# Kernel tuning notes

Measured on AMD Instinct MI355X. Metric: run time of the kernel, lower is better.

## Reference

```python
import jax, jax.numpy as jnp
import numpy as np

_EPS = 1e-6

def _warp_x(images, x_src):
    # images: [B,H,W,C]; x_src: [H,W] source x-coordinate for each output pixel
    # Nearest-neighbor resample along width, zero fill outside (tf ImageProjectiveTransform semantics).
    B, H, W, C = images.shape
    xi = jnp.round(x_src).astype(jnp.int32)
    valid = (xi >= 0) & (xi < W)
    xic = jnp.clip(xi, 0, W - 1)
    row = jnp.broadcast_to(jnp.arange(H)[:, None], (H, W))
    out = images[:, row, xic, :]  # gather -> [B,H,W,C]
    return out * valid[None, :, :, None].astype(images.dtype)

def _shear_x(images, mag):
    # transform matrix [1, mag, 0, 0, 1, 0]: x_in = x + mag * y
    H, W = images.shape[1], images.shape[2]
    yy = jnp.arange(H, dtype=jnp.float32)[:, None]
    xx = jnp.arange(W, dtype=jnp.float32)[None, :]
    return _warp_x(images, xx + mag * yy)

def _translate_x(images, pixels):
    # transform matrix [1, 0, -pixels, 0, 1, 0]: x_in = x - pixels
    H, W = images.shape[1], images.shape[2]
    xx = jnp.broadcast_to(jnp.arange(W, dtype=jnp.float32)[None, :], (H, W))
    return _warp_x(images, xx - pixels)

def _gumbel_softmax_hard(logits, u, tau=1.0):
    g = -jnp.log(-jnp.log(jnp.clip(u, _EPS, 1.0 - _EPS)))
    y = jax.nn.softmax((logits + g) / tau)
    onehot = jax.nn.one_hot(jnp.argmax(y), logits.shape[-1], dtype=y.dtype)
    return jax.lax.stop_gradient(onehot - y) + y  # straight-through hard sample

def _relaxed_bernoulli_hard(p, u, temperature=1.0):
    p = jnp.clip(p, _EPS, 1.0 - _EPS)
    l = jnp.log(jnp.clip(u, _EPS, 1.0 - _EPS)) - jnp.log1p(-jnp.clip(u, _EPS, 1.0 - _EPS))
    y = jax.nn.sigmoid((jnp.log(p) - jnp.log1p(-p) + l) / temperature)
    return jax.lax.stop_gradient(jnp.round(y) - y) + y  # straight-through hard sample

def _apply_bernoulli(x, op_fn, prob, magnitude, u_l):
    hw = _relaxed_bernoulli_hard(prob, u_l)
    x = x + magnitude - jax.lax.stop_gradient(magnitude)  # ST path for magnitude grad
    return jnp.where(hw == 1, op_fn(x, magnitude) * hw, x * (1 - hw))

def _forward(x, sp_weights, sp_probs, sp_magnitudes, u_gumbel, u_logistic):
    # sub-policy j=0: ShearX(-0.3, 0.3); j=1: TranslateX(-10, 10)
    ops = [
        lambda img, m: _shear_x(img, 0.6 * m - 0.3),
        lambda img, m: _translate_x(img, 20.0 * m - 10.0),
    ]
    num_ops, num_sp = sp_weights.shape
    for i in range(num_ops):
        hardwts = _gumbel_softmax_hard(sp_weights[i], u_gumbel[i])
        total = None
        for j in range(num_sp):
            term = jnp.where(
                hardwts[j] == 1,
                _apply_bernoulli(x, ops[j], sp_probs[i, j], sp_magnitudes[i, j], u_logistic[i, j]) * hardwts[j],
                hardwts[j],
            )
            total = term if total is None else total + term
        x = total
    return x

def setup_inputs() -> dict:
    key = jax.random.key(0)
    ks = jax.random.split(key, 6)
    x = jax.random.uniform(ks[0], (256, 224, 224, 3), dtype=jnp.float32)
    sp_weights = jax.random.uniform(ks[1], (2, 2), dtype=jnp.float32)
    sp_probs = jax.random.uniform(ks[2], (2, 2), dtype=jnp.float32)
    sp_magnitudes = jax.random.uniform(ks[3], (2, 2), dtype=jnp.float32)
    u_gumbel = jax.random.uniform(ks[4], (2, 2), dtype=jnp.float32)
    u_logistic = jax.random.uniform(ks[5], (2, 2), dtype=jnp.float32)
    return {"x": x, "sp_weights": sp_weights, "sp_probs": sp_probs,
            "sp_magnitudes": sp_magnitudes, "u_gumbel": u_gumbel, "u_logistic": u_logistic}

def reference(x, sp_weights, sp_probs, sp_magnitudes, u_gumbel, u_logistic):
    return _forward(x, sp_weights, sp_probs, sp_magnitudes, u_gumbel, u_logistic)
```

## Files before the change

kernel.cpp:

```cpp
#include <hip/hip_runtime.h>
#include <math.h>

#define EPS_F 1e-6f
#define CLIP_HI 0.999999f
#define IMG_W 224
#define IMG_H 224
#define ROWF (IMG_W * 3)

typedef float f32x4 __attribute__((ext_vector_type(4)));
typedef float f32x4_u __attribute__((ext_vector_type(4), aligned(4)));

__device__ __forceinline__ float clip01(float u) {
    return fminf(fmaxf(u, EPS_F), CLIP_HI);
}

__global__ void decide_kernel(const float* __restrict__ spw,
                              const float* __restrict__ spp,
                              const float* __restrict__ spm,
                              const float* __restrict__ ug,
                              const float* __restrict__ ul,
                              float* __restrict__ dec) {
    if (threadIdx.x != 0 || blockIdx.x != 0) return;
    for (int i = 0; i < 2; ++i) {
        float g0 = -logf(-logf(clip01(ug[i * 2 + 0])));
        float g1 = -logf(-logf(clip01(ug[i * 2 + 1])));
        int j = (spw[i * 2 + 0] + g0 >= spw[i * 2 + 1] + g1) ? 0 : 1;
        float p = clip01(spp[i * 2 + j]);
        float uc = clip01(ul[i * 2 + j]);
        float l = logf(uc) - log1pf(-uc);
        float s = (logf(p) - log1pf(-p)) + l;
        float y = 1.0f / (1.0f + expf(-s));
        int hw = (int)rintf(y);
        float m = spm[i * 2 + j];
        float active = 0.f, a = 0.f, b = 0.f;
        if (hw == 1) {
            active = 1.f;
            if (j == 0) {
                a = 0.6f * m - 0.3f;
            } else {
                b = -(20.0f * m - 10.0f);
            }
        }
        dec[i * 4 + 0] = active;
        dec[i * 4 + 1] = a;
        dec[i * 4 + 2] = b;
        dec[i * 4 + 3] = m;
    }
}

__global__ __launch_bounds__(256) void warp_kernel(const float* __restrict__ x,
                                                   const float* __restrict__ dec,
                                                   float* __restrict__ out,
                                                   int total_q) {
    int q = blockIdx.x * 256 + threadIdx.x;
    if (q >= total_q) return;
    int pos = q * 4;
    int row = pos / ROWF;
    int within = pos - row * ROWF;
    int h = row % IMG_H;
    int base = row * ROWF;

    const float a0 = dec[1], b0 = dec[2], m0 = dec[3];
    const float a1 = dec[5], b1 = dec[6], m1 = dec[7];
    const float hf = (float)h;
    const float sh1 = a1 * hf + b1;
    const float sh0 = a0 * hf + b0;

    int wA = within / 3;
    int cA = within - wA * 3;

    int x1A = (int)rintf((float)wA + sh1);
    bool vA = (x1A >= 0) && (x1A < IMG_W);
    int x0A = (int)rintf((float)x1A + sh0);
    vA = vA && (x0A >= 0) && (x0A < IMG_W);

    int x1B = (int)rintf((float)(wA + 1) + sh1);
    bool vB = (x1B >= 0) && (x1B < IMG_W);
    int x0B = (int)rintf((float)x1B + sh0);
    vB = vB && (x0B >= 0) && (x0B < IMG_W);

    bool fast = vA && vB && (x0B == x0A + 1);

    float r[4];
    if (__all(fast)) {
        const f32x4_u* src = reinterpret_cast<const f32x4_u*>(&x[base + 3 * x0A + cA]);
        f32x4_u v = *src;
#pragma unroll
        for (int e = 0; e < 4; ++e)
            r[e] = (((v[e] + m0) - m0) + m1) - m1;
    } else {
        int srcs[4];
        bool vs[4];
#pragma unroll
        for (int e = 0; e < 4; ++e) {
            int ce = cA + e;
            bool useB = (ce >= 3);
            int w0 = useB ? x0B : x0A;
            bool v = useB ? vB : vA;
            int cc = useB ? (ce - 3) : ce;
            int w0c = min(max(w0, 0), IMG_W - 1);
            srcs[e] = base + 3 * w0c + cc;
            vs[e] = v;
        }
        float vals[4];
#pragma unroll
        for (int e = 0; e < 4; ++e) vals[e] = x[srcs[e]];
#pragma unroll
        for (int e = 0; e < 4; ++e) {
            float t = vs[e] ? vals[e] : 0.f;
            t = (((t + m0) - m0) + m1) - m1;
            r[e] = vs[e] ? t : 0.f;
        }
    }

    f32x4 o = { r[0], r[1], r[2], r[3] };
    __builtin_nontemporal_store(o, reinterpret_cast<f32x4*>(&out[pos]));
}

extern "C" void kernel_launch(void* const* d_in, const int* in_sizes, int n_in,
                              void* d_out, int out_size, void* d_ws, size_t ws_size,
                              hipStream_t stream) {
    const float* x   = (const float*)d_in[0];
    const float* spw = (const float*)d_in[1];
    const float* spp = (const float*)d_in[2];
    const float* spm = (const float*)d_in[3];
    const float* ug  = (const float*)d_in[4];
    const float* ul  = (const float*)d_in[5];
    float* dec = (float*)d_ws;
    float* out = (float*)d_out;

    decide_kernel<<<1, 1, 0, stream>>>(spw, spp, spm, ug, ul, dec);

    int total_q = out_size / 4;
    int blocks = (total_q + 255) / 256;
    warp_kernel<<<blocks, 256, 0, stream>>>(x, dec, out, total_q);
}
```

Before: 56.71 us.

## Fuse decision computation into warp kernel and process two quads per thread

Removes the separate single-thread decide kernel. Each block's thread 0 now recomputes the sampling decisions into shared memory, followed by a block barrier. Each thread also handles two 4-float groups, one in each half of the output, which halves the grid size. This saves a kernel launch and its serialization, but every block now does redundant transcendental work and waits on a sync. The bounds check is gone, so the output size must divide evenly, which holds for this shape.

```diff
diff --git a/kernel.cpp b/kernel.cpp
--- a/kernel.cpp
+++ b/kernel.cpp
@@ -14,57 +14,17 @@
     return fminf(fmaxf(u, EPS_F), CLIP_HI);
 }
 
-__global__ void decide_kernel(const float* __restrict__ spw,
-                              const float* __restrict__ spp,
-                              const float* __restrict__ spm,
-                              const float* __restrict__ ug,
-                              const float* __restrict__ ul,
-                              float* __restrict__ dec) {
-    if (threadIdx.x != 0 || blockIdx.x != 0) return;
-    for (int i = 0; i < 2; ++i) {
-        float g0 = -logf(-logf(clip01(ug[i * 2 + 0])));
-        float g1 = -logf(-logf(clip01(ug[i * 2 + 1])));
-        int j = (spw[i * 2 + 0] + g0 >= spw[i * 2 + 1] + g1) ? 0 : 1;
-        float p = clip01(spp[i * 2 + j]);
-        float uc = clip01(ul[i * 2 + j]);
-        float l = logf(uc) - log1pf(-uc);
-        float s = (logf(p) - log1pf(-p)) + l;
-        float y = 1.0f / (1.0f + expf(-s));
-        int hw = (int)rintf(y);
-        float m = spm[i * 2 + j];
-        float active = 0.f, a = 0.f, b = 0.f;
-        if (hw == 1) {
-            active = 1.f;
-            if (j == 0) {
-                a = 0.6f * m - 0.3f;
-            } else {
-                b = -(20.0f * m - 10.0f);
-            }
-        }
-        dec[i * 4 + 0] = active;
-        dec[i * 4 + 1] = a;
-        dec[i * 4 + 2] = b;
-        dec[i * 4 + 3] = m;
-    }
-}
-
-__global__ __launch_bounds__(256) void warp_kernel(const float* __restrict__ x,
-                                                   const float* __restrict__ dec,
-                                                   float* __restrict__ out,
-                                                   int total_q) {
-    int q = blockIdx.x * 256 + threadIdx.x;
-    if (q >= total_q) return;
-    int pos = q * 4;
+__device__ __forceinline__ f32x4 process4(const float* __restrict__ x, int pos,
+                                          float sh0_a, float sh0_b,
+                                          float sh1_a, float sh1_b,
+                                          float m0, float m1) {
     int row = pos / ROWF;
     int within = pos - row * ROWF;
     int h = row % IMG_H;
     int base = row * ROWF;
-
-    const float a0 = dec[1], b0 = dec[2], m0 = dec[3];
-    const float a1 = dec[5], b1 = dec[6], m1 = dec[7];
-    const float hf = (float)h;
-    const float sh1 = a1 * hf + b1;
-    const float sh0 = a0 * hf + b0;
+    float hf = (float)h;
+    float sh1 = sh1_a * hf + sh1_b;
+    float sh0 = sh0_a * hf + sh0_b;
 
     int wA = within / 3;
     int cA = within - wA * 3;
@@ -81,13 +41,13 @@
 
     bool fast = vA && vB && (x0B == x0A + 1);
 
-    float r[4];
+    f32x4 o;
     if (__all(fast)) {
         const f32x4_u* src = reinterpret_cast<const f32x4_u*>(&x[base + 3 * x0A + cA]);
         f32x4_u v = *src;
 #pragma unroll
         for (int e = 0; e < 4; ++e)
-            r[e] = (((v[e] + m0) - m0) + m1) - m1;
+            o[e] = (((v[e] + m0) - m0) + m1) - m1;
     } else {
         int srcs[4];
         bool vs[4];
@@ -109,12 +69,58 @@
         for (int e = 0; e < 4; ++e) {
             float t = vs[e] ? vals[e] : 0.f;
             t = (((t + m0) - m0) + m1) - m1;
-            r[e] = vs[e] ? t : 0.f;
+            o[e] = vs[e] ? t : 0.f;
         }
     }
+    return o;
+}
 
-    f32x4 o = { r[0], r[1], r[2], r[3] };
-    __builtin_nontemporal_store(o, reinterpret_cast<f32x4*>(&out[pos]));
+__global__ __launch_bounds__(256) void warp_kernel(const float* __restrict__ x,
+                                                   const float* __restrict__ spw,
+                                                   const float* __restrict__ spp,
+                                                   const float* __restrict__ spm,
+                                                   const float* __restrict__ ug,
+                                                   const float* __restrict__ ul,
+                                                   float* __restrict__ out,
+                                                   int halfN) {
+    __shared__ float sdec[8];
+    if (threadIdx.x == 0) {
+#pragma unroll
+        for (int i = 0; i < 2; ++i) {
+            float g0 = -logf(-logf(clip01(ug[i * 2 + 0])));
+            float g1 = -logf(-logf(clip01(ug[i * 2 + 1])));
+            int j = (spw[i * 2 + 0] + g0 >= spw[i * 2 + 1] + g1) ? 0 : 1;
+            float p = clip01(spp[i * 2 + j]);
+            float uc = clip01(ul[i * 2 + j]);
+            float l = logf(uc) - log1pf(-uc);
+            float s = (logf(p) - log1pf(-p)) + l;
+            float y = 1.0f / (1.0f + expf(-s));
+            int hw = (int)rintf(y);
+            float m = spm[i * 2 + j];
+            float a = 0.f, b = 0.f;
+            if (hw == 1) {
+                if (j == 0) a = 0.6f * m - 0.3f;
+                else        b = -(20.0f * m - 10.0f);
+            }
+            sdec[i * 4 + 0] = a;
+            sdec[i * 4 + 1] = b;
+            sdec[i * 4 + 2] = m;
+            sdec[i * 4 + 3] = 0.f;
+        }
+    }
+    __syncthreads();
+    const float a0 = sdec[0], b0 = sdec[1], m0 = sdec[2];
+    const float a1 = sdec[4], b1 = sdec[5], m1 = sdec[6];
+
+    int q = blockIdx.x * 256 + threadIdx.x;
+    int pos0 = q * 4;
+    int pos1 = pos0 + halfN;
+
+    f32x4 o0 = process4(x, pos0, a0, b0, a1, b1, m0, m1);
+    f32x4 o1 = process4(x, pos1, a0, b0, a1, b1, m0, m1);
+
+    __builtin_nontemporal_store(o0, reinterpret_cast<f32x4*>(&out[pos0]));
+    __builtin_nontemporal_store(o1, reinterpret_cast<f32x4*>(&out[pos1]));
 }
 
 extern "C" void kernel_launch(void* const* d_in, const int* in_sizes, int n_in,
@@ -126,12 +132,10 @@
     const float* spm = (const float*)d_in[3];
     const float* ug  = (const float*)d_in[4];
     const float* ul  = (const float*)d_in[5];
-    float* dec = (float*)d_ws;
     float* out = (float*)d_out;
 
-    decide_kernel<<<1, 1, 0, stream>>>(spw, spp, spm, ug, ul, dec);
-
-    int total_q = out_size / 4;
-    int blocks = (total_q + 255) / 256;
-    warp_kernel<<<blocks, 256, 0, stream>>>(x, dec, out, total_q);
+    int halfN = out_size / 2;
+    int threads = out_size / 8;
+    int blocks = threads / 256;
+    warp_kernel<<<blocks, 256, 0, stream>>>(x, spw, spp, spm, ug, ul, out, halfN);
 }
```

Result: faster. 53.27 us (-6.1%).
